# Kernel optimization log

Measured on AMD Instinct MI355X. Metric: run time of the kernel, lower is better.

The kernel has to match this reference:

```python
import jax, jax.numpy as jnp
import numpy as np
from math import sqrt

EPS = 1e-8


def setup_inputs() -> dict:
    rng = jax.random.key(0)
    k1, k2, k3 = jax.random.split(rng, 3)
    BS, NA, NB, NK, NV = 16, 2048, 2048, 64, 64
    key = jax.random.normal(k1, (BS, NA, 1, NK), dtype=jnp.float32)
    query = jax.random.normal(k2, (BS, 1, NB, NK), dtype=jnp.float32)
    value = jax.random.normal(k3, (BS, NA, NV), dtype=jnp.float32)
    return {"key": key, "query": query, "value": value}


def reference(key, query, value):
    # key: (BS, NA, 1, NK); query: (BS, 1, NB, NK); value: (BS, NA, NV)
    NK = key.shape[-1]
    NV = value.shape[-1]
    BS, NB = query.shape[0], query.shape[2]
    # weights = sum(key * query, 3) / sqrt(NK)  -> (BS, NA, NB), via einsum
    w = jnp.einsum('bak,bnk->ban', key[:, :, 0, :], query[:, 0, :, :]) / sqrt(NK)
    # softmax over NA (dim 1), beta=1, drop=False
    w = jax.nn.softmax(w, axis=1)
    # values = sum_a w[b,a,n] * value[b,a,v] -> (BS, NB, NV)
    vals = jnp.einsum('ban,bav->bnv', w, value)
    # norm over feature dim (torch.std is unbiased, ddof=1)
    v2 = vals.reshape(BS * NB, NV)
    mu = v2.mean(axis=1, keepdims=True)
    std = v2.std(axis=1, keepdims=True, ddof=1)
    v2 = (v2 - mu) / (std + EPS)
    out = v2.reshape(BS, NB, NV).transpose(0, 2, 1)  # (BS, NV, NB)
    return out, w
```

## Files before the change

kernel.cpp:

```cpp
#include <hip/hip_runtime.h>
#include <math.h>

#define BS 16
#define NA 2048
#define NB 2048
#define NK 64
#define NV 64
#define EPS 1e-8f

typedef float        f32x4  __attribute__((ext_vector_type(4)));
typedef __bf16       bf16x8 __attribute__((ext_vector_type(8)));
typedef short        s16x8  __attribute__((ext_vector_type(8)));
typedef unsigned int u32x4  __attribute__((ext_vector_type(4)));
typedef unsigned short u16x8 __attribute__((ext_vector_type(8)));

template <typename V>
__device__ __forceinline__ auto mfma_impl(V a, V b, f32x4 c, int)
    -> decltype(__builtin_amdgcn_mfma_f32_16x16x32_bf16(a, b, c, 0, 0, 0)) {
    return __builtin_amdgcn_mfma_f32_16x16x32_bf16(a, b, c, 0, 0, 0);
}
template <typename V>
__device__ __forceinline__ auto mfma_impl(V a, V b, f32x4 c, long)
    -> decltype(__builtin_amdgcn_mfma_f32_16x16x32_bf16(
           __builtin_bit_cast(s16x8, a), __builtin_bit_cast(s16x8, b), c, 0, 0, 0)) {
    return __builtin_amdgcn_mfma_f32_16x16x32_bf16(
        __builtin_bit_cast(s16x8, a), __builtin_bit_cast(s16x8, b), c, 0, 0, 0);
}
__device__ __forceinline__ f32x4 mfma_bf16(u32x4 a, u32x4 b, f32x4 c) {
    bf16x8 av = __builtin_bit_cast(bf16x8, a);
    bf16x8 bv = __builtin_bit_cast(bf16x8, b);
    return mfma_impl(av, bv, c, 0);
}

__device__ __forceinline__ unsigned short f2bf(float x) {
    unsigned u = __builtin_bit_cast(unsigned, x);
    unsigned r = (u + 0x7FFFu + ((u >> 16) & 1u)) >> 16;
    return (unsigned short)r;
}
__device__ __forceinline__ u16x8 pk8(f32x4 a, f32x4 b) {
    u16x8 p;
    p[0] = f2bf(a[0]); p[1] = f2bf(a[1]); p[2] = f2bf(a[2]); p[3] = f2bf(a[3]);
    p[4] = f2bf(b[0]); p[5] = f2bf(b[1]); p[6] = f2bf(b[2]); p[7] = f2bf(b[3]);
    return p;
}
__device__ __forceinline__ f32x4 ldg4(const float* p) { return *(const f32x4*)p; }

__device__ __forceinline__ void bar_lgkm() {
    asm volatile("s_waitcnt lgkmcnt(0)" ::: "memory");
    __builtin_amdgcn_s_barrier();
}

__device__ __forceinline__ int swz128(int lin) {
    const int r = lin >> 7;
    const int c16 = (lin >> 4) & 7;
    return (r << 7) + ((c16 ^ (r & 7)) << 4) + (lin & 15);
}

__global__ __launch_bounds__(256)
void conv_bf16_kernel(const float* __restrict__ src, unsigned short* __restrict__ dst) {
    size_t i = ((size_t)blockIdx.x * 256 + threadIdx.x) * 8;
    f32x4 a = *(const f32x4*)(src + i);
    f32x4 b = *(const f32x4*)(src + i + 4);
    *(u16x8*)(dst + i) = pk8(a, b);
}

__global__ __launch_bounds__(256)
void transpose_v_kernel(const float* __restrict__ v, unsigned short* __restrict__ vt) {
    __shared__ float tile[64][65];
    const int b = blockIdx.y, at = blockIdx.x * 64;
    const float* Vb = v + (size_t)b * NA * NV;
    unsigned short* Vtb = vt + (size_t)b * NV * NA;
    const int r = threadIdx.x >> 2, c = (threadIdx.x & 3) * 16;
    #pragma unroll
    for (int j = 0; j < 4; ++j)
        *(f32x4*)&tile[r][c + 4 * j] = ldg4(Vb + (size_t)(at + r) * NV + c + 4 * j);
    __syncthreads();
    u16x8 p0, p1;
    #pragma unroll
    for (int j = 0; j < 8; ++j) p0[j] = f2bf(tile[c + j][r]);
    #pragma unroll
    for (int j = 0; j < 8; ++j) p1[j] = f2bf(tile[c + 8 + j][r]);
    *(u16x8*)(Vtb + (size_t)r * NA + at + c) = p0;
    *(u16x8*)(Vtb + (size_t)r * NA + at + c + 8) = p1;
}

#define BN2 32
#define NT  32
#define KD0 0
#define KD1 8192
#define VD0 16384
#define VD1 24576
#define ESB 32768
#define LRED 36864
#define LINV 37376
#define SMEMSZ 37504

__global__ __launch_bounds__(256, 4)
void attn_main2_kernel(const unsigned short* __restrict__ kb,
                       const unsigned short* __restrict__ qb,
                       const unsigned short* __restrict__ vtb,
                       float* __restrict__ out,
                       float* __restrict__ wout)
{
    __shared__ __align__(16) char smem[SMEMSZ];
    const int tid = threadIdx.x, w = tid >> 6, lane = tid & 63;
    const int lr = lane & 15, lg = lane >> 4;
    const int b = blockIdx.y, nb = blockIdx.x * BN2;

    const char* Kb = (const char*)(kb + (size_t)b * NA * NK);
    const char* Vt = (const char*)(vtb + (size_t)b * NV * NA);
    const unsigned short* Qb = qb + (size_t)b * NB * NK;
    float* Wb = wout + (size_t)b * NA * NB;
    float* Ob = out + (size_t)b * NV * NB;

    u32x4 af[2][2];
    #pragma unroll
    for (int t = 0; t < 2; ++t)
        #pragma unroll
        for (int c = 0; c < 2; ++c)
            af[t][c] = *(const u32x4*)&Qb[(size_t)(nb + t * 16 + lr) * NK + c * 32 + lg * 8];

    const int lin0 = tid * 16;
    const int lin1 = tid * 16 + 4096;
    const int kdst0 = swz128(lin0), kdst1 = swz128(lin1);
    const int vsrc0 = ((lin0 >> 7) * (NA * 2)) + (lin0 & 127);
    const int vsrc1 = ((lin1 >> 7) * (NA * 2)) + (lin1 & 127);

    const int row = w * 16 + lr;
    int kfro[2];
    #pragma unroll
    for (int c = 0; c < 2; ++c)
        kfro[c] = row * 128 + (((c * 4 + lg) ^ (row & 7)) << 4);
    int esro[2][2];
    #pragma unroll
    for (int t = 0; t < 2; ++t)
        #pragma unroll
        for (int c = 0; c < 2; ++c) {
            const int rr = t * 16 + lr;
            esro[t][c] = rr * 128 + (((c * 4 + lg) ^ (rr & 7)) << 4);
        }
    int eswo[2][4];
    #pragma unroll
    for (int t = 0; t < 2; ++t)
        #pragma unroll
        for (int r = 0; r < 4; ++r) {
            const int n = t * 16 + lg * 4 + r;
            eswo[t][r] = n * 128 + (((w * 2 + (lr >> 3)) ^ (n & 7)) << 4) + (lr & 7) * 2;
        }

    u32x4 kr0 = *(const u32x4*)(Kb + lin0);
    u32x4 kr1 = *(const u32x4*)(Kb + lin1);
    *(u32x4*)(smem + KD0 + kdst0) = kr0;
    *(u32x4*)(smem + KD0 + kdst1) = kr1;
    bar_lgkm();

    float lacc[2][4] = {};
    for (int i = 0; i < NT; ++i) {
        const int p = i & 1;
        if (i + 1 < NT) {
            kr0 = *(const u32x4*)(Kb + (i + 1) * 8192 + lin0);
            kr1 = *(const u32x4*)(Kb + (i + 1) * 8192 + lin1);
        }
        const char* kbuf = smem + (p ? KD1 : KD0);
        u32x4 kf0 = *(const u32x4*)(kbuf + kfro[0]);
        u32x4 kf1 = *(const u32x4*)(kbuf + kfro[1]);
        #pragma unroll
        for (int t = 0; t < 2; ++t) {
            f32x4 acc = {0.f, 0.f, 0.f, 0.f};
            acc = mfma_bf16(af[t][0], kf0, acc);
            acc = mfma_bf16(af[t][1], kf1, acc);
            #pragma unroll
            for (int r = 0; r < 4; ++r)
                lacc[t][r] += __expf(acc[r] * 0.125f);
        }
        if (i + 1 < NT) {
            char* kbn = smem + (p ? KD0 : KD1);
            *(u32x4*)(kbn + kdst0) = kr0;
            *(u32x4*)(kbn + kdst1) = kr1;
        }
        bar_lgkm();
    }

    #pragma unroll
    for (int t = 0; t < 2; ++t)
        #pragma unroll
        for (int r = 0; r < 4; ++r) {
            float v = lacc[t][r];
            v += __shfl_xor(v, 1); v += __shfl_xor(v, 2);
            v += __shfl_xor(v, 4); v += __shfl_xor(v, 8);
            lacc[t][r] = v;
        }
    if (lr == 0) {
        float* lp = (float*)(smem + LRED);
        #pragma unroll
        for (int t = 0; t < 2; ++t)
            #pragma unroll
            for (int r = 0; r < 4; ++r)
                lp[w * 32 + t * 16 + lg * 4 + r] = lacc[t][r];
    }
    __syncthreads();
    if (tid < 32) {
        const float* lp = (const float*)(smem + LRED);
        ((float*)(smem + LINV))[tid] =
            1.0f / (lp[tid] + lp[32 + tid] + lp[64 + tid] + lp[96 + tid]);
    }
    __syncthreads();
    f32x4 linv[2];
    linv[0] = *(const f32x4*)(smem + LINV + (lg * 4) * 4);
    linv[1] = *(const f32x4*)(smem + LINV + (16 + lg * 4) * 4);

    f32x4 pacc[2] = {{0.f,0.f,0.f,0.f},{0.f,0.f,0.f,0.f}};

    kr0 = *(const u32x4*)(Kb + lin0);
    kr1 = *(const u32x4*)(Kb + lin1);
    u32x4 vr0 = *(const u32x4*)(Vt + vsrc0);
    u32x4 vr1 = *(const u32x4*)(Vt + vsrc1);
    *(u32x4*)(smem + KD0 + kdst0) = kr0;
    *(u32x4*)(smem + KD0 + kdst1) = kr1;
    *(u32x4*)(smem + VD0 + kdst0) = vr0;
    *(u32x4*)(smem + VD0 + kdst1) = vr1;
    bar_lgkm();

    for (int i = 0; i < NT; ++i) {
        const int p = i & 1;
        if (i + 1 < NT) {
            kr0 = *(const u32x4*)(Kb + (i + 1) * 8192 + lin0);
            kr1 = *(const u32x4*)(Kb + (i + 1) * 8192 + lin1);
            vr0 = *(const u32x4*)(Vt + (i + 1) * 128 + vsrc0);
            vr1 = *(const u32x4*)(Vt + (i + 1) * 128 + vsrc1);
        }
        const char* kbuf = smem + (p ? KD1 : KD0);
        const char* vbuf = smem + (p ? VD1 : VD0);
        u32x4 kf0 = *(const u32x4*)(kbuf + kfro[0]);
        u32x4 kf1 = *(const u32x4*)(kbuf + kfro[1]);
        const int at = i * 64;
        #pragma unroll
        for (int t = 0; t < 2; ++t) {
            f32x4 acc = {0.f, 0.f, 0.f, 0.f};
            acc = mfma_bf16(af[t][0], kf0, acc);
            acc = mfma_bf16(af[t][1], kf1, acc);
            f32x4 wv;
            #pragma unroll
            for (int r = 0; r < 4; ++r)
                wv[r] = __expf(acc[r] * 0.125f) * linv[t][r];
            *(f32x4*)(Wb + (size_t)(at + row) * NB + nb + t * 16 + lg * 4) = wv;
            #pragma unroll
            for (int r = 0; r < 4; ++r)
                *(unsigned short*)(smem + ESB + eswo[t][r]) = f2bf(wv[r]);
        }
        bar_lgkm();

        u32x4 pa[2][2];
        #pragma unroll
        for (int t = 0; t < 2; ++t)
            #pragma unroll
            for (int c = 0; c < 2; ++c)
                pa[t][c] = *(const u32x4*)(smem + ESB + esro[t][c]);
        u32x4 vf0 = *(const u32x4*)(vbuf + kfro[0]);
        u32x4 vf1 = *(const u32x4*)(vbuf + kfro[1]);
        #pragma unroll
        for (int t = 0; t < 2; ++t) {
            pacc[t] = mfma_bf16(pa[t][0], vf0, pacc[t]);
            pacc[t] = mfma_bf16(pa[t][1], vf1, pacc[t]);
        }
        if (i + 1 < NT) {
            char* kbn = smem + (p ? KD0 : KD1);
            char* vbn = smem + (p ? VD0 : VD1);
            *(u32x4*)(kbn + kdst0) = kr0;
            *(u32x4*)(kbn + kdst1) = kr1;
            *(u32x4*)(vbn + kdst0) = vr0;
            *(u32x4*)(vbn + kdst1) = vr1;
        }
        bar_lgkm();
    }

    __syncthreads();
    float* vals = (float*)smem;
    #pragma unroll
    for (int t = 0; t < 2; ++t)
        #pragma unroll
        for (int r = 0; r < 4; ++r)
            vals[(t * 16 + lg * 4 + r) * 66 + w * 16 + lr] = pacc[t][r];
    __syncthreads();
    {
        const int n = tid >> 3, v0 = (tid & 7) * 8;
        float sv[8], s1 = 0.f, s2 = 0.f;
        #pragma unroll
        for (int j = 0; j < 8; ++j) {
            float x = vals[n * 66 + v0 + j];
            sv[j] = x; s1 += x; s2 = fmaf(x, x, s2);
        }
        s1 += __shfl_xor(s1, 1); s2 += __shfl_xor(s2, 1);
        s1 += __shfl_xor(s1, 2); s2 += __shfl_xor(s2, 2);
        s1 += __shfl_xor(s1, 4); s2 += __shfl_xor(s2, 4);
        const float mu = s1 * (1.0f / 64.0f);
        float var = (s2 - 64.0f * mu * mu) * (1.0f / 63.0f);
        var = fmaxf(var, 0.0f);
        const float istd = 1.0f / (sqrtf(var) + EPS);
        #pragma unroll
        for (int j = 0; j < 8; ++j)
            vals[n * 66 + v0 + j] = (sv[j] - mu) * istd;
    }
    __syncthreads();
    {
        const int v = tid >> 2, q = (tid & 3) * 8;
        f32x4 o0, o1;
        #pragma unroll
        for (int j = 0; j < 4; ++j) o0[j] = vals[(q + j) * 66 + v];
        #pragma unroll
        for (int j = 0; j < 4; ++j) o1[j] = vals[(q + 4 + j) * 66 + v];
        *(f32x4*)(Ob + (size_t)v * NB + nb + q) = o0;
        *(f32x4*)(Ob + (size_t)v * NB + nb + q + 4) = o1;
    }
}

#define SQ 72
#define OSTR 68
#define SMEM_BYTES 38144

__global__ __launch_bounds__(256, 2)
void attn_fb_kernel(const float* __restrict__ key, const float* __restrict__ query,
                    const float* __restrict__ value, float* __restrict__ out,
                    float* __restrict__ wout)
{
    __shared__ __align__(16) char smem[SMEM_BYTES];
    unsigned short* Qs = (unsigned short*)(smem);
    unsigned short* Ks = (unsigned short*)(smem + 9216);
    unsigned short* Vts = (unsigned short*)(smem + 18432);
    unsigned short* Es = (unsigned short*)(smem + 27648);
    float* linv_s = (float*)(smem + 36864);
    float (*lred)[64] = (float (*)[64])(smem + 37120);
    float* outl = (float*)(smem + 18432);

    const int tid = threadIdx.x, wave = tid >> 6, lane = tid & 63;
    const int lr = lane & 15, lg = lane >> 4;
    const int b = blockIdx.y, nb = blockIdx.x * 64, aw = wave * 16;

    const float* Kb = key + (size_t)b * NA * NK;
    const float* Qb = query + (size_t)b * NB * NK;
    const float* Vb = value + (size_t)b * NA * NV;
    float* Wb = wout + (size_t)b * NA * NB;
    float* Ob = out + (size_t)b * NV * NB;

    {
        const int r = tid >> 2, c = (tid & 3) * 16;
        const float* src = Qb + (size_t)(nb + r) * NK + c;
        f32x4 q0 = ldg4(src), q1 = ldg4(src + 4), q2 = ldg4(src + 8), q3 = ldg4(src + 12);
        *(u16x8*)&Qs[r * SQ + c] = pk8(q0, q1);
        *(u16x8*)&Qs[r * SQ + c + 8] = pk8(q2, q3);
    }
    float lacc[4][4] = {};
    for (int at = 0; at < NA; at += 64) {
        {
            const int r = tid >> 2, c = (tid & 3) * 16;
            const float* src = Kb + (size_t)(at + r) * NK + c;
            f32x4 k0 = ldg4(src), k1 = ldg4(src + 4), k2 = ldg4(src + 8), k3 = ldg4(src + 12);
            *(u16x8*)&Ks[r * SQ + c] = pk8(k0, k1);
            *(u16x8*)&Ks[r * SQ + c + 8] = pk8(k2, k3);
        }
        __syncthreads();
        u32x4 bf0 = *(const u32x4*)&Ks[(aw + lr) * SQ + (lg * 8)];
        u32x4 bf1 = *(const u32x4*)&Ks[(aw + lr) * SQ + (32 + lg * 8)];
        #pragma unroll
        for (int t = 0; t < 4; ++t) {
            f32x4 acc = {0.f, 0.f, 0.f, 0.f};
            u32x4 af0 = *(const u32x4*)&Qs[(t * 16 + lr) * SQ + (lg * 8)];
            u32x4 af1 = *(const u32x4*)&Qs[(t * 16 + lr) * SQ + (32 + lg * 8)];
            acc = mfma_bf16(af0, bf0, acc);
            acc = mfma_bf16(af1, bf1, acc);
            #pragma unroll
            for (int r = 0; r < 4; ++r) lacc[t][r] += __expf(acc[r] * 0.125f);
        }
        __syncthreads();
    }
    #pragma unroll
    for (int t = 0; t < 4; ++t)
        #pragma unroll
        for (int r = 0; r < 4; ++r) {
            float v = lacc[t][r];
            v += __shfl_xor(v, 1); v += __shfl_xor(v, 2);
            v += __shfl_xor(v, 4); v += __shfl_xor(v, 8);
            lacc[t][r] = v;
        }
    if (lr == 0)
        #pragma unroll
        for (int t = 0; t < 4; ++t)
            #pragma unroll
            for (int r = 0; r < 4; ++r)
                lred[wave][t * 16 + lg * 4 + r] = lacc[t][r];
    __syncthreads();
    if (tid < 64) {
        float s = lred[0][tid] + lred[1][tid] + lred[2][tid] + lred[3][tid];
        linv_s[tid] = 1.0f / s;
    }
    __syncthreads();
    f32x4 linv[4];
    #pragma unroll
    for (int t = 0; t < 4; ++t) linv[t] = *(const f32x4*)&linv_s[t * 16 + lg * 4];

    f32x4 pacc[4] = {{0.f,0.f,0.f,0.f},{0.f,0.f,0.f,0.f},{0.f,0.f,0.f,0.f},{0.f,0.f,0.f,0.f}};
    for (int at = 0; at < NA; at += 64) {
        {
            const int r = tid >> 2, c = (tid & 3) * 16;
            const float* src = Kb + (size_t)(at + r) * NK + c;
            f32x4 k0 = ldg4(src), k1 = ldg4(src + 4), k2 = ldg4(src + 8), k3 = ldg4(src + 12);
            *(u16x8*)&Ks[r * SQ + c] = pk8(k0, k1);
            *(u16x8*)&Ks[r * SQ + c + 8] = pk8(k2, k3);
        }
        {
            const int ap = (tid & 31) * 2, q = tid >> 5;
            const float* v0p = Vb + (size_t)(at + ap) * NV + q * 8;
            const float* v1p = v0p + NV;
            f32x4 a0 = ldg4(v0p), a1 = ldg4(v0p + 4);
            f32x4 b0 = ldg4(v1p), b1 = ldg4(v1p + 4);
            #pragma unroll
            for (int j = 0; j < 4; ++j) {
                unsigned int w0 = (unsigned)f2bf(a0[j]) | ((unsigned)f2bf(b0[j]) << 16);
                *(unsigned int*)&Vts[(q * 8 + j) * SQ + ap] = w0;
                unsigned int w1 = (unsigned)f2bf(a1[j]) | ((unsigned)f2bf(b1[j]) << 16);
                *(unsigned int*)&Vts[(q * 8 + 4 + j) * SQ + ap] = w1;
            }
        }
        __syncthreads();
        u32x4 bf0 = *(const u32x4*)&Ks[(aw + lr) * SQ + (lg * 8)];
        u32x4 bf1 = *(const u32x4*)&Ks[(aw + lr) * SQ + (32 + lg * 8)];
        #pragma unroll
        for (int t = 0; t < 4; ++t) {
            f32x4 acc = {0.f, 0.f, 0.f, 0.f};
            u32x4 af0 = *(const u32x4*)&Qs[(t * 16 + lr) * SQ + (lg * 8)];
            u32x4 af1 = *(const u32x4*)&Qs[(t * 16 + lr) * SQ + (32 + lg * 8)];
            acc = mfma_bf16(af0, bf0, acc);
            acc = mfma_bf16(af1, bf1, acc);
            f32x4 wv;
            #pragma unroll
            for (int r = 0; r < 4; ++r) wv[r] = __expf(acc[r] * 0.125f) * linv[t][r];
            *(f32x4*)(Wb + (size_t)(at + aw + lr) * NB + nb + t * 16 + lg * 4) = wv;
            #pragma unroll
            for (int r = 0; r < 4; ++r)
                Es[(t * 16 + lg * 4 + r) * SQ + (aw + lr)] = f2bf(wv[r]);
        }
        __syncthreads();
        u32x4 paf0 = *(const u32x4*)&Es[(wave * 16 + lr) * SQ + (lg * 8)];
        u32x4 paf1 = *(const u32x4*)&Es[(wave * 16 + lr) * SQ + (32 + lg * 8)];
        #pragma unroll
        for (int t = 0; t < 4; ++t) {
            u32x4 vb0 = *(const u32x4*)&Vts[(t * 16 + lr) * SQ + (lg * 8)];
            u32x4 vb1 = *(const u32x4*)&Vts[(t * 16 + lr) * SQ + (32 + lg * 8)];
            pacc[t] = mfma_bf16(paf0, vb0, pacc[t]);
            pacc[t] = mfma_bf16(paf1, vb1, pacc[t]);
        }
        __syncthreads();
    }
    float mu[4], istd[4];
    #pragma unroll
    for (int r = 0; r < 4; ++r) {
        float s1 = 0.f, s2 = 0.f;
        #pragma unroll
        for (int t = 0; t < 4; ++t) { float x = pacc[t][r]; s1 += x; s2 = fmaf(x, x, s2); }
        s1 += __shfl_xor(s1, 1); s2 += __shfl_xor(s2, 1);
        s1 += __shfl_xor(s1, 2); s2 += __shfl_xor(s2, 2);
        s1 += __shfl_xor(s1, 4); s2 += __shfl_xor(s2, 4);
        s1 += __shfl_xor(s1, 8); s2 += __shfl_xor(s2, 8);
        float m = s1 * (1.0f / 64.0f);
        float var = (s2 - 64.0f * m * m) * (1.0f / 63.0f);
        var = fmaxf(var, 0.0f);
        mu[r] = m; istd[r] = 1.0f / (sqrtf(var) + EPS);
    }
    #pragma unroll
    for (int t = 0; t < 4; ++t)
        #pragma unroll
        for (int r = 0; r < 4; ++r)
            outl[(t * 16 + lr) * OSTR + wave * 16 + lg * 4 + r] = (pacc[t][r] - mu[r]) * istd[r];
    __syncthreads();
    {
        const int v = tid >> 2, c = (tid & 3) * 16;
        float* dst = Ob + (size_t)v * NB + nb + c;
        const float* srcr = &outl[v * OSTR + c];
        #pragma unroll
        for (int j = 0; j < 4; ++j)
            *(f32x4*)(dst + 4 * j) = *(const f32x4*)(srcr + 4 * j);
    }
}

extern "C" void kernel_launch(void* const* d_in, const int* in_sizes, int n_in,
                              void* d_out, int out_size, void* d_ws, size_t ws_size,
                              hipStream_t stream) {
    const float* key   = (const float*)d_in[0];
    const float* query = (const float*)d_in[1];
    const float* value = (const float*)d_in[2];
    float* out  = (float*)d_out;
    float* wout = out + (size_t)BS * NV * NB;

    const size_t elems = (size_t)BS * NA * NK;
    const size_t need = 3 * elems * sizeof(unsigned short);
    if (ws_size >= need) {
        unsigned short* kb = (unsigned short*)d_ws;
        unsigned short* qb = kb + elems;
        unsigned short* vt = qb + elems;
        conv_bf16_kernel<<<dim3((unsigned)(elems / (256 * 8))), 256, 0, stream>>>(key, kb);
        conv_bf16_kernel<<<dim3((unsigned)(elems / (256 * 8))), 256, 0, stream>>>(query, qb);
        transpose_v_kernel<<<dim3(NA / 64, BS), 256, 0, stream>>>(value, vt);
        attn_main2_kernel<<<dim3(NB / BN2, BS), 256, 0, stream>>>(kb, qb, vt, out, wout);
    } else {
        attn_fb_kernel<<<dim3(NB / 64, BS), 256, 0, stream>>>(key, query, value, out, wout);
    }
}
```

Measured before the change: 97.25 us.

## Single-buffer LDS tiles, swizzle block order, add setprio and nontemporal weight stores

Shrinks shared memory from double-buffered K/V tiles to single buffers in the second pass, cutting the LDS footprint roughly in half so more blocks can be resident per CU. Block indices are remapped to a 1D grid with a swizzle that spreads batches across XCDs or L2 partitions. It also adds s_setprio around MFMA regions, uses nontemporal stores for the large attention-weight output, and uses the native bf16 conversion. The cost is that single buffering puts loads and compute in the same buffer within an iteration, which serialises them more, and the swizzle changes cache locality for K and V.

```diff
diff --git a/kernel.cpp b/kernel.cpp
--- a/kernel.cpp
+++ b/kernel.cpp
@@ -86,17 +86,15 @@
 
 #define BN2 32
 #define NT  32
-#define KD0 0
-#define KD1 8192
-#define VD0 16384
-#define VD1 24576
-#define ESB 32768
-#define LRED 36864
-#define LINV 37376
-#define SMEMSZ 37504
+#define KD  0
+#define VD  8192
+#define ESB 16384
+#define LRED 20480
+#define LINV 20992
+#define SMEMSZ 21120
 
 __global__ __launch_bounds__(256, 4)
-void attn_main2_kernel(const unsigned short* __restrict__ kb,
+void attn_main3_kernel(const unsigned short* __restrict__ kb,
                        const unsigned short* __restrict__ qb,
                        const unsigned short* __restrict__ vtb,
                        float* __restrict__ out,
@@ -105,7 +103,10 @@
     __shared__ __align__(16) char smem[SMEMSZ];
     const int tid = threadIdx.x, w = tid >> 6, lane = tid & 63;
     const int lr = lane & 15, lg = lane >> 4;
-    const int b = blockIdx.y, nb = blockIdx.x * BN2;
+
+    const int lin = blockIdx.x;
+    const int swz = (lin & 7) * 128 + (lin >> 3);
+    const int b = swz >> 6, nb = (swz & 63) * BN2;
 
     const char* Kb = (const char*)(kb + (size_t)b * NA * NK);
     const char* Vt = (const char*)(vtb + (size_t)b * NV * NA);
@@ -148,55 +149,59 @@
             eswo[t][r] = n * 128 + (((w * 2 + (lr >> 3)) ^ (n & 7)) << 4) + (lr & 7) * 2;
         }
 
-    u32x4 kr0 = *(const u32x4*)(Kb + lin0);
-    u32x4 kr1 = *(const u32x4*)(Kb + lin1);
-    *(u32x4*)(smem + KD0 + kdst0) = kr0;
-    *(u32x4*)(smem + KD0 + kdst1) = kr1;
-    bar_lgkm();
-
-    float lacc[2][4] = {};
-    for (int i = 0; i < NT; ++i) {
-        const int p = i & 1;
-        if (i + 1 < NT) {
-            kr0 = *(const u32x4*)(Kb + (i + 1) * 8192 + lin0);
-            kr1 = *(const u32x4*)(Kb + (i + 1) * 8192 + lin1);
-        }
-        const char* kbuf = smem + (p ? KD1 : KD0);
-        u32x4 kf0 = *(const u32x4*)(kbuf + kfro[0]);
-        u32x4 kf1 = *(const u32x4*)(kbuf + kfro[1]);
-        #pragma unroll
-        for (int t = 0; t < 2; ++t) {
-            f32x4 acc = {0.f, 0.f, 0.f, 0.f};
-            acc = mfma_bf16(af[t][0], kf0, acc);
-            acc = mfma_bf16(af[t][1], kf1, acc);
-            #pragma unroll
-            for (int r = 0; r < 4; ++r)
-                lacc[t][r] += __expf(acc[r] * 0.125f);
-        }
-        if (i + 1 < NT) {
-            char* kbn = smem + (p ? KD0 : KD1);
-            *(u32x4*)(kbn + kdst0) = kr0;
-            *(u32x4*)(kbn + kdst1) = kr1;
-        }
+    {
+        u32x4 kr0 = *(const u32x4*)(Kb + lin0);
+        u32x4 kr1 = *(const u32x4*)(Kb + lin1);
+        *(u32x4*)(smem + KD + kdst0) = kr0;
+        *(u32x4*)(smem + KD + kdst1) = kr1;
         bar_lgkm();
-    }
-
-    #pragma unroll
-    for (int t = 0; t < 2; ++t)
-        #pragma unroll
-        for (int r = 0; r < 4; ++r) {
-            float v = lacc[t][r];
-            v += __shfl_xor(v, 1); v += __shfl_xor(v, 2);
-            v += __shfl_xor(v, 4); v += __shfl_xor(v, 8);
-            lacc[t][r] = v;
-        }
-    if (lr == 0) {
-        float* lp = (float*)(smem + LRED);
+
+        float lacc[2][4] = {};
+        for (int i = 0; i < NT; ++i) {
+            const int p = i & 1;
+            if (i + 1 < NT) {
+                kr0 = *(const u32x4*)(Kb + (i + 1) * 8192 + lin0);
+                kr1 = *(const u32x4*)(Kb + (i + 1) * 8192 + lin1);
+            }
+            const char* kbuf = smem + (p ? VD : KD);
+            u32x4 kf0 = *(const u32x4*)(kbuf + kfro[0]);
+            u32x4 kf1 = *(const u32x4*)(kbuf + kfro[1]);
+            __builtin_amdgcn_s_setprio(1);
+            #pragma unroll
+            for (int t = 0; t < 2; ++t) {
+                f32x4 acc = {0.f, 0.f, 0.f, 0.f};
+                acc = mfma_bf16(af[t][0], kf0, acc);
+                acc = mfma_bf16(af[t][1], kf1, acc);
+                #pragma unroll
+                for (int r = 0; r < 4; ++r)
+                    lacc[t][r] += __expf(acc[r] * 0.125f);
+            }
+            __builtin_amdgcn_s_setprio(0);
+            if (i + 1 < NT) {
+                char* kbn = smem + (p ? KD : VD);
+                *(u32x4*)(kbn + kdst0) = kr0;
+                *(u32x4*)(kbn + kdst1) = kr1;
+            }
+            bar_lgkm();
+        }
+
         #pragma unroll
         for (int t = 0; t < 2; ++t)
             #pragma unroll
-            for (int r = 0; r < 4; ++r)
-                lp[w * 32 + t * 16 + lg * 4 + r] = lacc[t][r];
+            for (int r = 0; r < 4; ++r) {
+                float v = lacc[t][r];
+                v += __shfl_xor(v, 1); v += __shfl_xor(v, 2);
+                v += __shfl_xor(v, 4); v += __shfl_xor(v, 8);
+                lacc[t][r] = v;
+            }
+        if (lr == 0) {
+            float* lp = (float*)(smem + LRED);
+            #pragma unroll
+            for (int t = 0; t < 2; ++t)
+                #pragma unroll
+                for (int r = 0; r < 4; ++r)
+                    lp[w * 32 + t * 16 + lg * 4 + r] = lacc[t][r];
+        }
     }
     __syncthreads();
     if (tid < 32) {
@@ -211,67 +216,72 @@
 
     f32x4 pacc[2] = {{0.f,0.f,0.f,0.f},{0.f,0.f,0.f,0.f}};
 
-    kr0 = *(const u32x4*)(Kb + lin0);
-    kr1 = *(const u32x4*)(Kb + lin1);
-    u32x4 vr0 = *(const u32x4*)(Vt + vsrc0);
-    u32x4 vr1 = *(const u32x4*)(Vt + vsrc1);
-    *(u32x4*)(smem + KD0 + kdst0) = kr0;
-    *(u32x4*)(smem + KD0 + kdst1) = kr1;
-    *(u32x4*)(smem + VD0 + kdst0) = vr0;
-    *(u32x4*)(smem + VD0 + kdst1) = vr1;
-    bar_lgkm();
-
-    for (int i = 0; i < NT; ++i) {
-        const int p = i & 1;
-        if (i + 1 < NT) {
-            kr0 = *(const u32x4*)(Kb + (i + 1) * 8192 + lin0);
-            kr1 = *(const u32x4*)(Kb + (i + 1) * 8192 + lin1);
-            vr0 = *(const u32x4*)(Vt + (i + 1) * 128 + vsrc0);
-            vr1 = *(const u32x4*)(Vt + (i + 1) * 128 + vsrc1);
-        }
-        const char* kbuf = smem + (p ? KD1 : KD0);
-        const char* vbuf = smem + (p ? VD1 : VD0);
-        u32x4 kf0 = *(const u32x4*)(kbuf + kfro[0]);
-        u32x4 kf1 = *(const u32x4*)(kbuf + kfro[1]);
-        const int at = i * 64;
-        #pragma unroll
-        for (int t = 0; t < 2; ++t) {
-            f32x4 acc = {0.f, 0.f, 0.f, 0.f};
-            acc = mfma_bf16(af[t][0], kf0, acc);
-            acc = mfma_bf16(af[t][1], kf1, acc);
-            f32x4 wv;
-            #pragma unroll
-            for (int r = 0; r < 4; ++r)
-                wv[r] = __expf(acc[r] * 0.125f) * linv[t][r];
-            *(f32x4*)(Wb + (size_t)(at + row) * NB + nb + t * 16 + lg * 4) = wv;
-            #pragma unroll
-            for (int r = 0; r < 4; ++r)
-                *(unsigned short*)(smem + ESB + eswo[t][r]) = f2bf(wv[r]);
-        }
+    {
+        u32x4 kr0 = *(const u32x4*)(Kb + lin0);
+        u32x4 kr1 = *(const u32x4*)(Kb + lin1);
+        u32x4 vr0 = *(const u32x4*)(Vt + vsrc0);
+        u32x4 vr1 = *(const u32x4*)(Vt + vsrc1);
+        *(u32x4*)(smem + KD + kdst0) = kr0;
+        *(u32x4*)(smem + KD + kdst1) = kr1;
+        *(u32x4*)(smem + VD + kdst0) = vr0;
+        *(u32x4*)(smem + VD + kdst1) = vr1;
         bar_lgkm();
 
-        u32x4 pa[2][2];
-        #pragma unroll
-        for (int t = 0; t < 2; ++t)
-            #pragma unroll
-            for (int c = 0; c < 2; ++c)
-                pa[t][c] = *(const u32x4*)(smem + ESB + esro[t][c]);
-        u32x4 vf0 = *(const u32x4*)(vbuf + kfro[0]);
-        u32x4 vf1 = *(const u32x4*)(vbuf + kfro[1]);
-        #pragma unroll
-        for (int t = 0; t < 2; ++t) {
-            pacc[t] = mfma_bf16(pa[t][0], vf0, pacc[t]);
-            pacc[t] = mfma_bf16(pa[t][1], vf1, pacc[t]);
-        }
-        if (i + 1 < NT) {
-            char* kbn = smem + (p ? KD0 : KD1);
-            char* vbn = smem + (p ? VD0 : VD1);
-            *(u32x4*)(kbn + kdst0) = kr0;
-            *(u32x4*)(kbn + kdst1) = kr1;
-            *(u32x4*)(vbn + kdst0) = vr0;
-            *(u32x4*)(vbn + kdst1) = vr1;
-        }
-        bar_lgkm();
+        for (int i = 0; i < NT; ++i) {
+            if (i + 1 < NT) {
+                kr0 = *(const u32x4*)(Kb + (i + 1) * 8192 + lin0);
+                kr1 = *(const u32x4*)(Kb + (i + 1) * 8192 + lin1);
+                vr0 = *(const u32x4*)(Vt + (i + 1) * 128 + vsrc0);
+                vr1 = *(const u32x4*)(Vt + (i + 1) * 128 + vsrc1);
+            }
+            u32x4 kf0 = *(const u32x4*)(smem + KD + kfro[0]);
+            u32x4 kf1 = *(const u32x4*)(smem + KD + kfro[1]);
+            u32x4 vf0 = *(const u32x4*)(smem + VD + kfro[0]);
+            u32x4 vf1 = *(const u32x4*)(smem + VD + kfro[1]);
+            const int at = i * 64;
+            __builtin_amdgcn_s_setprio(1);
+            #pragma unroll
+            for (int t = 0; t < 2; ++t) {
+                f32x4 acc = {0.f, 0.f, 0.f, 0.f};
+                acc = mfma_bf16(af[t][0], kf0, acc);
+                acc = mfma_bf16(af[t][1], kf1, acc);
+                f32x4 wv;
+                #pragma unroll
+                for (int r = 0; r < 4; ++r)
+                    wv[r] = __expf(acc[r] * 0.125f) * linv[t][r];
+                __builtin_nontemporal_store(
+                    wv, (f32x4*)(Wb + (size_t)(at + row) * NB + nb + t * 16 + lg * 4));
+                #pragma unroll
+                for (int r = 0; r < 4; ++r) {
+                    __bf16 e = (__bf16)wv[r];
+                    *(unsigned short*)(smem + ESB + eswo[t][r]) =
+                        __builtin_bit_cast(unsigned short, e);
+                }
+            }
+            __builtin_amdgcn_s_setprio(0);
+            bar_lgkm();
+
+            u32x4 pa[2][2];
+            #pragma unroll
+            for (int t = 0; t < 2; ++t)
+                #pragma unroll
+                for (int c = 0; c < 2; ++c)
+                    pa[t][c] = *(const u32x4*)(smem + ESB + esro[t][c]);
+            __builtin_amdgcn_s_setprio(1);
+            #pragma unroll
+            for (int t = 0; t < 2; ++t) {
+                pacc[t] = mfma_bf16(pa[t][0], vf0, pacc[t]);
+                pacc[t] = mfma_bf16(pa[t][1], vf1, pacc[t]);
+            }
+            __builtin_amdgcn_s_setprio(0);
+            if (i + 1 < NT) {
+                *(u32x4*)(smem + KD + kdst0) = kr0;
+                *(u32x4*)(smem + KD + kdst1) = kr1;
+                *(u32x4*)(smem + VD + kdst0) = vr0;
+                *(u32x4*)(smem + VD + kdst1) = vr1;
+            }
+            bar_lgkm();
+        }
     }
 
     __syncthreads();
@@ -500,7 +510,7 @@
         conv_bf16_kernel<<<dim3((unsigned)(elems / (256 * 8))), 256, 0, stream>>>(key, kb);
         conv_bf16_kernel<<<dim3((unsigned)(elems / (256 * 8))), 256, 0, stream>>>(query, qb);
         transpose_v_kernel<<<dim3(NA / 64, BS), 256, 0, stream>>>(value, vt);
-        attn_main2_kernel<<<dim3(NB / BN2, BS), 256, 0, stream>>>(kb, qb, vt, out, wout);
+        attn_main3_kernel<<<dim3(1024), 256, 0, stream>>>(kb, qb, vt, out, wout);
     } else {
         attn_fb_kernel<<<dim3(NB / 64, BS), 256, 0, stream>>>(key, query, value, out, wout);
     }
```

After: 106.2 us. +9.2%, slower.
